# Kernel tuning notes

Measured on AMD Instinct MI355X. Metric: run time of the kernel, lower is better.

The kernel has to match this reference:

```python
import jax, jax.numpy as jnp
import numpy as np

EPS = 1e-12  # matches torch F.normalize / CosineSimilarity eps scale (1e-12 / 1e-8; vectors are unit so effect is negligible)


def setup_inputs() -> dict:
    key = jax.random.key(0)
    X = jax.random.normal(key, (64, 1024, 128), dtype=jnp.float32)
    return {"X": X}


def reference(X) -> jnp.ndarray:
    # F.normalize(X, dim=-1)
    Xn = X / jnp.maximum(jnp.linalg.norm(X, axis=-1, keepdims=True), EPS)
    # CosineSimilarity on unit vectors == batched X @ X^T  -> [B, scale, scale]
    S = jnp.einsum("bsd,btd->bst", Xn, Xn)
    # MSE vs ones per batch, averaged over batch == global mean of (S-1)^2
    return jnp.mean((S - 1.0) ** 2)
```

## Files before the change

### kernel.cpp

```cpp
#include <hip/hip_runtime.h>
#include <hip/hip_bf16.h>


#define BATCH 64
#define SEQ   1024
#define DIM   128

typedef short short8  __attribute__((ext_vector_type(8)));
typedef float floatx4 __attribute__((ext_vector_type(4)));

__device__ __forceinline__ unsigned bf16rne(float x) {
    unsigned u = __builtin_bit_cast(unsigned, x);
    return (u + 0x7FFFu + ((u >> 16) & 1u)) >> 16;
}

#define XNT_B  0
#define VP_B   16777216
#define RES_B  (VP_B + 512 * 256 * 4)


__global__ __launch_bounds__(256, 2)
void kA_norm_t(const float* __restrict__ X, unsigned* __restrict__ XnT,
               float* __restrict__ vpartA) {
    __shared__ __align__(16) float lds[64][132];
    const int t    = threadIdx.x;
    const int wg   = blockIdx.x;
    const int b    = wg & 63, sblk = wg >> 6;
    const int sl   = t >> 2, q = t & 3;
    const int f    = t & 127, sh = t >> 7;
    const int rb   = f >> 4, l15 = f & 15;

    float4 g[2][8];
#pragma unroll
    for (int c = 0; c < 2; ++c) {
        const float4* rp = (const float4*)(
            X + ((size_t)(b * SEQ + sblk * 128 + c * 64 + sl) * DIM + q * 32));
#pragma unroll
        for (int k = 0; k < 8; ++k) g[c][k] = rp[k];
    }

    float vacc = 0.0f;
#pragma unroll
    for (int c = 0; c < 2; ++c) {
        float ssq = 0.0f;
#pragma unroll
        for (int k = 0; k < 8; ++k)
            ssq += g[c][k].x * g[c][k].x + g[c][k].y * g[c][k].y +
                   g[c][k].z * g[c][k].z + g[c][k].w * g[c][k].w;
        ssq += __shfl_xor(ssq, 1);
        ssq += __shfl_xor(ssq, 2);
        const float inv = rsqrtf(fmaxf(ssq, 1e-24f));

        if (c) __syncthreads();
#pragma unroll
        for (int k = 0; k < 8; ++k) {
            float4 n;
            n.x = g[c][k].x * inv; n.y = g[c][k].y * inv;
            n.z = g[c][k].z * inv; n.w = g[c][k].w * inv;
            *(float4*)&lds[sl][q * 32 + k * 4] = n;
        }
        __syncthreads();

        float v[32];
#pragma unroll
        for (int j = 0; j < 32; ++j) {
            v[j] = lds[sh * 32 + j][f];
            vacc += v[j];
        }
        unsigned pk[16];
#pragma unroll
        for (int p = 0; p < 16; ++p)
            pk[p] = bf16rne(v[2 * p]) | (bf16rne(v[2 * p + 1]) << 16);

        const int kk = sblk * 4 + c * 2 + sh;
        uint4* op = (uint4*)(XnT + (((size_t)((b * 8 + rb) * 32 + kk)) << 8));
#pragma unroll
        for (int k = 0; k < 4; ++k)
            op[k * 16 + l15] = make_uint4(pk[4 * k], pk[4 * k + 1],
                                          pk[4 * k + 2], pk[4 * k + 3]);
    }
    vpartA[(size_t)wg * 256 + t] = vacc;
}

__global__ __launch_bounds__(256, 2)
void kB_gram(const unsigned* __restrict__ XnT, const float* __restrict__ vpartA,
             float* __restrict__ res) {
    const int t    = threadIdx.x;
    const int wg   = blockIdx.x;
    const int b    = wg & 63, band = wg >> 6;
    const int lane = t & 63, w = t >> 6;

    const unsigned* Ab  = XnT + (((size_t)((b * 8 + band) * 32)) << 8) + lane * 4;
    const unsigned* B0b = XnT + (((size_t)((b * 8 + 2 * w) * 32)) << 8) + lane * 4;
    const unsigned* B1b = XnT + (((size_t)((b * 8 + 2 * w + 1) * 32)) << 8) + lane * 4;

    floatx4 acc0 = {0.f, 0.f, 0.f, 0.f}, acc1 = {0.f, 0.f, 0.f, 0.f};
#pragma unroll 8
    for (int kk = 0; kk < 32; ++kk) {
        short8 a  = *(const short8*)(Ab  + (kk << 8));
        short8 b0 = *(const short8*)(B0b + (kk << 8));
        short8 b1 = *(const short8*)(B1b + (kk << 8));
        acc0 = __builtin_amdgcn_mfma_f32_16x16x32_bf16(a, b0, acc0, 0, 0, 0);
        acc1 = __builtin_amdgcn_mfma_f32_16x16x32_bf16(a, b1, acc1, 0, 0, 0);
    }

    float s = acc0[0] * acc0[0] + acc0[1] * acc0[1] +
              acc0[2] * acc0[2] + acc0[3] * acc0[3] +
              acc1[0] * acc1[0] + acc1[1] * acc1[1] +
              acc1[2] * acc1[2] + acc1[3] * acc1[3];

    if (band == 0 && t < DIM) {
        float vv = 0.0f;
#pragma unroll
        for (int sblk = 0; sblk < 8; ++sblk) {
            const float* p = vpartA + (size_t)(sblk * 64 + b) * 256;
            vv += p[t] + p[t + 128];
        }
        s -= 2.0f * vv * vv;
    }

#pragma unroll
    for (int m = 1; m < 64; m <<= 1) s += __shfl_xor(s, m);
    __shared__ float wq[4];
    if (lane == 0) wq[w] = s;
    __syncthreads();
    if (t == 0) res[wg] = wq[0] + wq[1] + wq[2] + wq[3];
}

__global__ __launch_bounds__(256)
void kF_final(const float* __restrict__ res, float* __restrict__ out) {
    const int t = threadIdx.x;
    float s = res[t] + res[t + 256];
#pragma unroll
    for (int m = 1; m < 64; m <<= 1) s += __shfl_xor(s, m);
    __shared__ float wq[4];
    if ((t & 63) == 0) wq[t >> 6] = s;
    __syncthreads();
    if (t == 0)
        out[0] = (wq[0] + wq[1] + wq[2] + wq[3]) * (1.0f / 67108864.0f) + 1.0f;
}

extern "C" void kernel_launch(void* const* d_in, const int* in_sizes, int n_in,
                              void* d_out, int out_size, void* d_ws, size_t ws_size,
                              hipStream_t stream) {
    const float* X = (const float*)d_in[0];
    char* ws = (char*)d_ws;
    unsigned* XnT  = (unsigned*)(ws + XNT_B);
    float* vpartA  = (float*)(ws + VP_B);
    float* res     = (float*)(ws + RES_B);

    kA_norm_t<<<512, 256, 0, stream>>>(X, XnT, vpartA);
    kB_gram<<<512, 256, 0, stream>>>(XnT, vpartA, res);
    kF_final<<<1, 256, 0, stream>>>(res, (float*)d_out);
}
```

Baseline: 86.85 us.

## Split normalize kernel into more blocks, pad LDS, fuse final reduce via atomic counter

The normalize/transpose kernel now runs twice as many workgroups, each handling 64 rows instead of 128, with launch bounds raised to 4 waves per SIMD for more parallelism and latency hiding. The LDS tile is padded per 32-column group to reduce bank conflicts on the transposed reads. The separate final-reduction kernel is removed: the last Gram workgroup, detected with an atomic counter, performs the final sum, saving a kernel launch. The counter is reset inside the first kernel, which relies on stream ordering, and the vpart workspace grows to match.

```diff
diff --git a/kernel.cpp b/kernel.cpp
--- a/kernel.cpp
+++ b/kernel.cpp
@@ -16,75 +16,74 @@
 
 #define XNT_B  0
 #define VP_B   16777216
-#define RES_B  (VP_B + 512 * 256 * 4)
+#define RES_B  (VP_B + 1024 * 256 * 4)
+#define CNT_B  (RES_B + 512 * 4)
 
 
-__global__ __launch_bounds__(256, 2)
+__global__ __launch_bounds__(256, 4)
 void kA_norm_t(const float* __restrict__ X, unsigned* __restrict__ XnT,
-               float* __restrict__ vpartA) {
-    __shared__ __align__(16) float lds[64][132];
-    const int t    = threadIdx.x;
-    const int wg   = blockIdx.x;
-    const int b    = wg & 63, sblk = wg >> 6;
-    const int sl   = t >> 2, q = t & 3;
-    const int f    = t & 127, sh = t >> 7;
-    const int rb   = f >> 4, l15 = f & 15;
+               float* __restrict__ vpartA, int* __restrict__ counter) {
+    __shared__ __align__(16) float lds[64][140];
+    const int t     = threadIdx.x;
+    const int wg    = blockIdx.x;
+    const int b     = wg & 63, chunk = wg >> 6;
+    const int sl    = t >> 2, q = t & 3;
+    const int f     = t & 127, sh = t >> 7;
+    const int rb    = f >> 4, l15 = f & 15;
 
-    float4 g[2][8];
+    if (wg == 0 && t == 0) *counter = 0;
+
+    const float4* rp = (const float4*)(
+        X + ((size_t)(b * SEQ + chunk * 64 + sl) * DIM + q * 32));
+    float4 g[8];
 #pragma unroll
-    for (int c = 0; c < 2; ++c) {
-        const float4* rp = (const float4*)(
-            X + ((size_t)(b * SEQ + sblk * 128 + c * 64 + sl) * DIM + q * 32));
+    for (int k = 0; k < 8; ++k) g[k] = rp[k];
+
+    float ssq = 0.0f;
 #pragma unroll
-        for (int k = 0; k < 8; ++k) g[c][k] = rp[k];
+    for (int k = 0; k < 8; ++k)
+        ssq += g[k].x * g[k].x + g[k].y * g[k].y +
+               g[k].z * g[k].z + g[k].w * g[k].w;
+    ssq += __shfl_xor(ssq, 1);
+    ssq += __shfl_xor(ssq, 2);
+    const float inv = rsqrtf(fmaxf(ssq, 1e-24f));
+
+#pragma unroll
+    for (int k = 0; k < 8; ++k) {
+        float4 n;
+        n.x = g[k].x * inv; n.y = g[k].y * inv;
+        n.z = g[k].z * inv; n.w = g[k].w * inv;
+        *(float4*)&lds[sl][q * 36 + k * 4] = n;
     }
+    __syncthreads();
 
+    const int fcol = (f >> 5) * 36 + (f & 31);
     float vacc = 0.0f;
+    float v[32];
 #pragma unroll
-    for (int c = 0; c < 2; ++c) {
-        float ssq = 0.0f;
+    for (int j = 0; j < 32; ++j) {
+        v[j] = lds[sh * 32 + j][fcol];
+        vacc += v[j];
+    }
+    unsigned pk[16];
 #pragma unroll
-        for (int k = 0; k < 8; ++k)
-            ssq += g[c][k].x * g[c][k].x + g[c][k].y * g[c][k].y +
-                   g[c][k].z * g[c][k].z + g[c][k].w * g[c][k].w;
-        ssq += __shfl_xor(ssq, 1);
-        ssq += __shfl_xor(ssq, 2);
-        const float inv = rsqrtf(fmaxf(ssq, 1e-24f));
+    for (int p = 0; p < 16; ++p)
+        pk[p] = bf16rne(v[2 * p]) | (bf16rne(v[2 * p + 1]) << 16);
 
-        if (c) __syncthreads();
+    const int kk = chunk * 2 + sh;
+    uint4* op = (uint4*)(XnT + (((size_t)((b * 8 + rb) * 32 + kk)) << 8));
 #pragma unroll
-        for (int k = 0; k < 8; ++k) {
-            float4 n;
-            n.x = g[c][k].x * inv; n.y = g[c][k].y * inv;
-            n.z = g[c][k].z * inv; n.w = g[c][k].w * inv;
-            *(float4*)&lds[sl][q * 32 + k * 4] = n;
-        }
-        __syncthreads();
+    for (int k = 0; k < 4; ++k)
+        op[k * 16 + l15] = make_uint4(pk[4 * k], pk[4 * k + 1],
+                                      pk[4 * k + 2], pk[4 * k + 3]);
 
-        float v[32];
-#pragma unroll
-        for (int j = 0; j < 32; ++j) {
-            v[j] = lds[sh * 32 + j][f];
-            vacc += v[j];
-        }
-        unsigned pk[16];
-#pragma unroll
-        for (int p = 0; p < 16; ++p)
-            pk[p] = bf16rne(v[2 * p]) | (bf16rne(v[2 * p + 1]) << 16);
-
-        const int kk = sblk * 4 + c * 2 + sh;
-        uint4* op = (uint4*)(XnT + (((size_t)((b * 8 + rb) * 32 + kk)) << 8));
-#pragma unroll
-        for (int k = 0; k < 4; ++k)
-            op[k * 16 + l15] = make_uint4(pk[4 * k], pk[4 * k + 1],
-                                          pk[4 * k + 2], pk[4 * k + 3]);
-    }
     vpartA[(size_t)wg * 256 + t] = vacc;
 }
 
 __global__ __launch_bounds__(256, 2)
 void kB_gram(const unsigned* __restrict__ XnT, const float* __restrict__ vpartA,
-             float* __restrict__ res) {
+             float* __restrict__ res, int* __restrict__ counter,
+             float* __restrict__ out) {
     const int t    = threadIdx.x;
     const int wg   = blockIdx.x;
     const int b    = wg & 63, band = wg >> 6;
@@ -112,8 +111,8 @@
     if (band == 0 && t < DIM) {
         float vv = 0.0f;
 #pragma unroll
-        for (int sblk = 0; sblk < 8; ++sblk) {
-            const float* p = vpartA + (size_t)(sblk * 64 + b) * 256;
+        for (int c = 0; c < 16; ++c) {
+            const float* p = vpartA + (size_t)(c * 64 + b) * 256;
             vv += p[t] + p[t + 128];
         }
         s -= 2.0f * vv * vv;
@@ -122,22 +121,26 @@
 #pragma unroll
     for (int m = 1; m < 64; m <<= 1) s += __shfl_xor(s, m);
     __shared__ float wq[4];
+    __shared__ int lastflag;
     if (lane == 0) wq[w] = s;
     __syncthreads();
-    if (t == 0) res[wg] = wq[0] + wq[1] + wq[2] + wq[3];
-}
-
-__global__ __launch_bounds__(256)
-void kF_final(const float* __restrict__ res, float* __restrict__ out) {
-    const int t = threadIdx.x;
-    float s = res[t] + res[t + 256];
+    if (t == 0) {
+        res[wg] = wq[0] + wq[1] + wq[2] + wq[3];
+        __threadfence();
+        lastflag = (atomicAdd(counter, 1) == 511);
+    }
+    __syncthreads();
+    if (lastflag) {
+        __threadfence();
+        float s2 = res[t] + res[t + 256];
 #pragma unroll
-    for (int m = 1; m < 64; m <<= 1) s += __shfl_xor(s, m);
-    __shared__ float wq[4];
-    if ((t & 63) == 0) wq[t >> 6] = s;
-    __syncthreads();
-    if (t == 0)
-        out[0] = (wq[0] + wq[1] + wq[2] + wq[3]) * (1.0f / 67108864.0f) + 1.0f;
+        for (int m = 1; m < 64; m <<= 1) s2 += __shfl_xor(s2, m);
+        if ((t & 63) == 0) wq[t >> 6] = s2;
+        __syncthreads();
+        if (t == 0)
+            out[0] = (wq[0] + wq[1] + wq[2] + wq[3]) * (1.0f / 67108864.0f)
+                     + 1.0f;
+    }
 }
 
 extern "C" void kernel_launch(void* const* d_in, const int* in_sizes, int n_in,
@@ -148,8 +151,8 @@
     unsigned* XnT  = (unsigned*)(ws + XNT_B);
     float* vpartA  = (float*)(ws + VP_B);
     float* res     = (float*)(ws + RES_B);
+    int*   counter = (int*)(ws + CNT_B);
 
-    kA_norm_t<<<512, 256, 0, stream>>>(X, XnT, vpartA);
-    kB_gram<<<512, 256, 0, stream>>>(XnT, vpartA, res);
-    kF_final<<<1, 256, 0, stream>>>(res, (float*)d_out);
+    kA_norm_t<<<1024, 256, 0, stream>>>(X, XnT, vpartA, counter);
+    kB_gram<<<512, 256, 0, stream>>>(XnT, vpartA, res, counter, (float*)d_out);
 }
```

Measured after the change: 93.14 us. 7.2% more time.
